# Performance work log

Hardware: AMD Instinct MI355X
Metric: run time of the kernel (lower is better)

The kernel has to match this reference:

```python
import jax, jax.numpy as jnp
import numpy as np

N = 200000      # tweet nodes
E = 1600000     # edges
U = 20000       # users (num_users)
D = 64          # embedding_dimension1 == embedding_dimension2
NUMP, CATP = 20, 12
EPS = 0.1       # PyG FAConv default eps


def setup_inputs() -> dict:
    key = jax.random.key(0)
    ks = jax.random.split(key, 20)
    s = 0.05
    offs = jnp.sort(jax.random.randint(ks[3], (U + 1,), 0, N, dtype=jnp.int64))
    offs = offs.at[0].set(0).at[-1].set(N)
    return {
        "num_prop": jax.random.normal(ks[0], (N, NUMP), jnp.float32),
        "cat_prop": jax.random.normal(ks[1], (N, CATP), jnp.float32),
        "tweet_offsets": offs,
        "edge_index": jax.random.randint(ks[2], (2, E), 0, N, dtype=jnp.int64),
        "re_index": jax.random.randint(ks[4], (U,), 0, U, dtype=jnp.int64),
        "W_num": jax.random.normal(ks[5], (NUMP, D // 2), jnp.float32) * s,
        "b_num": jnp.zeros((D // 2,), jnp.float32),
        "W_cat": jax.random.normal(ks[6], (CATP, D // 2), jnp.float32) * s,
        "b_cat": jnp.zeros((D // 2,), jnp.float32),
        "W_tog": jax.random.normal(ks[7], (D, D), jnp.float32) * s,
        "b_tog": jnp.zeros((D,), jnp.float32),
        "att_l": jax.random.normal(ks[8], (D,), jnp.float32) * s,
        "att_r": jax.random.normal(ks[9], (D,), jnp.float32) * s,
        "W_f1": jax.random.normal(ks[10], (D, D // 2), jnp.float32) * s,
        "b_f1": jnp.zeros((D // 2,), jnp.float32),
        "W_lab": jax.random.normal(ks[11], (D // 2, 2), jnp.float32) * s,
        "b_lab": jnp.zeros((2,), jnp.float32),
    }


def reference(num_prop, cat_prop, tweet_offsets, edge_index, re_index,
              W_num, b_num, W_cat, b_cat, W_tog, b_tog,
              att_l, att_r, W_f1, b_f1, W_lab, b_lab):
    n = num_prop.shape[0]
    lrelu = jax.nn.leaky_relu  # slope 0.01, matches nn.LeakyReLU default

    num = lrelu(num_prop @ W_num + b_num)
    cat = lrelu(cat_prop @ W_cat + b_cat)
    x = lrelu(jnp.concatenate([num, cat], axis=1) @ W_tog + b_tog)  # [N, D]

    # gcn_norm with self-loops (PyG FAConv default normalize=True, add_self_loops=True)
    loop = jnp.arange(n, dtype=edge_index.dtype)
    src = jnp.concatenate([edge_index[0], loop])
    dst = jnp.concatenate([edge_index[1], loop])
    deg = jax.ops.segment_sum(jnp.ones(src.shape[0], jnp.float32), dst, num_segments=n)
    dinv = jnp.where(deg > 0, deg ** -0.5, 0.0)
    norm = dinv[src] * dinv[dst]  # [E+N]

    def faconv(h, h0):
        # alpha_e = tanh(att_l . h[src] + att_r . h[dst]); out_i = sum_e norm_e * alpha_e * h[src_e]
        al = h @ att_l
        ar = h @ att_r
        alpha = jnp.tanh(al[src] + ar[dst]) * norm
        agg = jax.ops.segment_sum(h[src] * alpha[:, None], dst, num_segments=n)
        return agg + EPS * h0

    x1 = faconv(x, x)      # dropout is identity in eval mode
    x2 = faconv(x1, x)
    x2 = jnp.sqrt(x2 ** 2 + 1e-8)

    # ragged per-user segment sum from CSR offsets (replaces python loop+slice)
    nseg = tweet_offsets.shape[0] - 1
    seg = jnp.searchsorted(tweet_offsets, jnp.arange(n), side='right') - 1
    seg = jnp.clip(seg, 0, nseg - 1)
    x3 = jax.ops.segment_sum(x2, seg, num_segments=nseg)  # [U, D]

    x3 = x3[re_index]
    h = lrelu(x3 @ W_f1 + b_f1)
    return h @ W_lab + b_lab
```

## Files before the change

kernel.cpp:

```cpp
#include <hip/hip_runtime.h>
#include <hip/hip_bf16.h>

#define LRELU(v) ((v) > 0.0f ? (v) : 0.01f * (v))
#define EPS 0.1f

#define BSHIFT  9
#define BSIZE   512
#define BIN_EPB 2048
#define BIN_CAP 6144

typedef __attribute__((ext_vector_type(8))) short bf16x8;
typedef __attribute__((ext_vector_type(4))) float f32x4;

__device__ __forceinline__ float fast_tanh(float v)
{
    float e = __expf(2.0f * v);
    return 1.0f - 2.0f * __builtin_amdgcn_rcpf(e + 1.0f);
}

__device__ __forceinline__ float bf2f(unsigned short h)
{
    return __uint_as_float(((unsigned int)h) << 16);
}
__device__ __forceinline__ unsigned short f2bf(float f)
{
    unsigned int u = __float_as_uint(f);
    u += 0x7FFFu + ((u >> 16) & 1u);
    return (unsigned short)(u >> 16);
}

__global__ void k_prep(const float* __restrict__ W_num, const float* __restrict__ W_cat,
                       const float* __restrict__ W_tog,
                       unsigned short* __restrict__ Wb, unsigned short* __restrict__ Wb1)
{
    int t = threadIdx.x;
    for (int i = t; i < 8 * 512; i += 256) {
        int tile = i >> 9;
        int kt   = tile >> 2, nt = tile & 3;
        int lane = (i >> 3) & 63;
        int j    = i & 7;
        int k    = kt * 32 + (lane >> 4) * 8 + j;
        int n    = nt * 16 + (lane & 15);
        Wb[i] = f2bf(W_tog[k * 64 + n]);
    }
    for (int i = t; i < 4 * 512; i += 256) {
        int nt   = i >> 9;
        int lane = (i >> 3) & 63;
        int j    = i & 7;
        int k    = (lane >> 4) * 8 + j;
        int n    = nt * 16 + (lane & 15);
        float w;
        if (n < 32) w = (k < 20)  ? W_num[k * 32 + n]              : 0.0f;
        else        w = (k >= 20) ? W_cat[(k - 20) * 32 + (n - 32)] : 0.0f;
        Wb1[i] = f2bf(w);
    }
}

__global__ void __launch_bounds__(256)
k_feat(const float* __restrict__ num_prop,
       const float* __restrict__ cat_prop,
       const unsigned short* __restrict__ Wb1,
       const float* __restrict__ b_num, const float* __restrict__ b_cat,
       const unsigned short* __restrict__ Wb, const float* __restrict__ b_tog,
       const float* __restrict__ att_l, const float* __restrict__ att_r,
       unsigned short* __restrict__ xb,
       float* __restrict__ al, float* __restrict__ ar, int N)
{
    __shared__ unsigned short in_lds[64][40];
    __shared__ unsigned short mid[64][72];

    int tid  = threadIdx.x;
    int lane = tid & 63;
    int w    = tid >> 6;
    int blockStart = blockIdx.x * 64;

    for (int i = tid; i < 64 * 20; i += 256) {
        int node = i / 20, k = i % 20;
        int n = min(blockStart + node, N - 1);
        in_lds[node][k] = f2bf(num_prop[(size_t)n * 20 + k]);
    }
    for (int i = tid; i < 64 * 12; i += 256) {
        int node = i / 12, k = i % 12;
        int n = min(blockStart + node, N - 1);
        in_lds[node][20 + k] = f2bf(cat_prop[(size_t)n * 12 + k]);
    }
    __syncthreads();

    int q   = lane >> 4;
    int c16 = lane & 15;

    bf16x8 ain = *(const bf16x8*)&in_lds[w * 16 + c16][q * 8];
    #pragma unroll
    for (int nt = 0; nt < 4; nt++) {
        bf16x8 b = *(const bf16x8*)&Wb1[nt * 512 + lane * 8];
        f32x4 acc = {0.0f, 0.0f, 0.0f, 0.0f};
        acc = __builtin_amdgcn_mfma_f32_16x16x32_bf16(ain, b, acc, 0, 0, 0);
        int   ch   = nt * 16 + c16;
        float bias = (ch < 32) ? b_num[ch] : b_cat[ch - 32];
        #pragma unroll
        for (int r = 0; r < 4; r++) {
            float s = acc[r] + bias;
            s = LRELU(s);
            mid[w * 16 + q * 4 + r][ch] = f2bf(s);
        }
    }

    bf16x8 a0 = *(const bf16x8*)&mid[w * 16 + c16][q * 8];
    bf16x8 a1 = *(const bf16x8*)&mid[w * 16 + c16][32 + q * 8];

    float pal[4] = {0, 0, 0, 0};
    float par[4] = {0, 0, 0, 0};

    #pragma unroll
    for (int nt = 0; nt < 4; nt++) {
        bf16x8 b0 = *(const bf16x8*)&Wb[(0 * 4 + nt) * 512 + lane * 8];
        bf16x8 b1 = *(const bf16x8*)&Wb[(1 * 4 + nt) * 512 + lane * 8];
        f32x4 acc = {0.0f, 0.0f, 0.0f, 0.0f};
        acc = __builtin_amdgcn_mfma_f32_16x16x32_bf16(a0, b0, acc, 0, 0, 0);
        acc = __builtin_amdgcn_mfma_f32_16x16x32_bf16(a1, b1, acc, 0, 0, 0);

        int   ch  = nt * 16 + c16;
        float bt  = b_tog[ch];
        float atl = att_l[ch];
        float atr = att_r[ch];
        #pragma unroll
        for (int r = 0; r < 4; r++) {
            float s = acc[r] + bt;
            s = LRELU(s);
            int n = blockStart + w * 16 + q * 4 + r;
            if (n < N) xb[(size_t)n * 64 + ch] = f2bf(s);
            pal[r] = fmaf(s, atl, pal[r]);
            par[r] = fmaf(s, atr, par[r]);
        }
    }

    #pragma unroll
    for (int r = 0; r < 4; r++) {
        float pl = pal[r], pr = par[r];
        #pragma unroll
        for (int off = 8; off > 0; off >>= 1) {
            pl += __shfl_xor(pl, off);
            pr += __shfl_xor(pr, off);
        }
        int n = blockStart + w * 16 + q * 4 + r;
        if (c16 == 0 && n < N) { al[n] = pl; ar[n] = pr; }
    }
}

__global__ void k_bin(const int* __restrict__ src, const int* __restrict__ dst,
                      int* __restrict__ bucket_cnt,
                      int2* __restrict__ buckets, int E, int NB)
{
    __shared__ int  hist[BSIZE];
    __shared__ int  lbase[BSIZE];
    __shared__ int  gbase[BSIZE];
    __shared__ int2 stage[BIN_EPB];

    int tid  = threadIdx.x;
    int base = blockIdx.x * BIN_EPB;

    hist[tid] = 0;
    __syncthreads();

    int s[4], d[4], rk[4];
    #pragma unroll
    for (int k = 0; k < 4; k++) {
        int e = base + k * BSIZE + tid;
        s[k] = -1;
        if (e < E) {
            s[k] = src[e];
            d[k] = dst[e];
            rk[k] = atomicAdd(&hist[d[k] >> BSHIFT], 1);
        }
    }
    __syncthreads();

    int v = hist[tid];
    lbase[tid] = v;
    __syncthreads();
    for (int off = 1; off < BSIZE; off <<= 1) {
        int t = (tid >= off) ? lbase[tid - off] : 0;
        __syncthreads();
        lbase[tid] += t;
        __syncthreads();
    }
    int incl = lbase[tid];
    __syncthreads();
    lbase[tid] = incl - v;
    if (tid < NB && v > 0) gbase[tid] = atomicAdd(&bucket_cnt[tid], v);
    __syncthreads();

    #pragma unroll
    for (int k = 0; k < 4; k++) {
        if (s[k] >= 0) {
            int b = d[k] >> BSHIFT;
            stage[lbase[b] + rk[k]] = make_int2(s[k], d[k]);
        }
    }
    __syncthreads();

    int tot = min(BIN_EPB, E - base);
    for (int i = tid; i < tot; i += BSIZE) {
        int2 p = stage[i];
        int b = p.y >> BSHIFT;
        buckets[(size_t)b * BIN_CAP + gbase[b] + (i - lbase[b])] = p;
    }
}

__global__ void k_degScan(const int2* __restrict__ buckets, const int* __restrict__ bucket_cnt,
                          int* __restrict__ deg, int* __restrict__ row_start,
                          int* __restrict__ bucketTot, int N)
{
    __shared__ int cnt[BSIZE];
    __shared__ int sc[BSIZE];
    int b   = blockIdx.x;
    int tid = threadIdx.x;
    cnt[tid] = 0;
    __syncthreads();

    int ecnt = bucket_cnt[b];
    const int2* bp = buckets + (size_t)b * BIN_CAP;
    for (int i = tid; i < ecnt; i += BSIZE)
        atomicAdd(&cnt[bp[i].y & (BSIZE - 1)], 1);
    __syncthreads();

    int d = cnt[tid];
    int p = (d + 7) & ~7;
    sc[tid] = p;
    __syncthreads();
    for (int off = 1; off < BSIZE; off <<= 1) {
        int t = (tid >= off) ? sc[tid - off] : 0;
        __syncthreads();
        sc[tid] += t;
        __syncthreads();
    }
    int incl = sc[tid];

    int n = b * BSIZE + tid;
    if (n < N) {
        deg[n]       = d;
        row_start[n] = incl - p;
    }
    if (tid == BSIZE - 1) bucketTot[b] = incl;
}

__global__ void k_scan2(int* __restrict__ bucketTot, int nb)
{
    __shared__ int sh[BSIZE];
    int tid = threadIdx.x;
    int v = (tid < nb) ? bucketTot[tid] : 0;
    sh[tid] = v;
    __syncthreads();
    for (int off = 1; off < BSIZE; off <<= 1) {
        int t = (tid >= off) ? sh[tid - off] : 0;
        __syncthreads();
        sh[tid] += t;
        __syncthreads();
    }
    if (tid < nb) bucketTot[tid] = sh[tid] - v;
}

__global__ void k_scan3(int* __restrict__ row_start, const int* __restrict__ bucketTot,
                        const int* __restrict__ deg,
                        const float* __restrict__ al, float2* __restrict__ ald1,
                        int* __restrict__ srcs, float* __restrict__ alphas,
                        const int* __restrict__ offs, int* __restrict__ seg,
                        int N, int U)
{
    int i = blockIdx.x * blockDim.x + threadIdx.x;
    if (i >= N) return;
    int s0 = row_start[i] + bucketTot[i >> BSHIFT];
    row_start[i] = s0;
    int cnt  = deg[i];
    int cntp = (cnt + 7) & ~7;
    for (int k = cnt; k < cntp; k++) {
        srcs[s0 + k]   = 0;
        alphas[s0 + k] = 0.0f;
    }
    float dv = 1.0f / sqrtf((float)cnt + 1.0f);
    ald1[i]  = make_float2(al[i], dv);

    int lo = 0, hi = U;
    while (lo < hi) {
        int mid = (lo + hi) >> 1;
        if (offs[mid] <= i) lo = mid + 1; else hi = mid;
    }
    seg[i] = min(max(lo - 1, 0), U - 1);
}

__global__ void k_fill2(const int2* __restrict__ buckets, const int* __restrict__ bucket_cnt,
                        const int* __restrict__ row_start,
                        const float2* __restrict__ ald, const float* __restrict__ arr,
                        int* __restrict__ srcs, float* __restrict__ alphas)
{
    __shared__ int cur[BSIZE];
    int b   = blockIdx.x;
    int tid = threadIdx.x;
    cur[tid] = 0;
    __syncthreads();

    int cnt = bucket_cnt[b];
    const int2* bp = buckets + (size_t)b * BIN_CAP;
    for (int i = tid; i < cnt; i += BSIZE) {
        int2 p = bp[i];
        int r = p.y & (BSIZE - 1);
        int o = atomicAdd(&cur[r], 1);
        int pos = row_start[p.y] + o;
        float2 as = ald[p.x];
        float2 ad = ald[p.y];
        srcs[pos]   = p.x;
        alphas[pos] = fast_tanh(as.x + arr[p.y]) * as.y * ad.y;
    }
}

__global__ void k_alphaN(const int* __restrict__ srcs,
                         const int* __restrict__ row_start, const int* __restrict__ deg,
                         const float2* __restrict__ ald, const float* __restrict__ arr,
                         float* __restrict__ alphas, int N)
{
    int n = blockIdx.x * blockDim.x + threadIdx.x;
    if (n >= N) return;
    int   s0   = row_start[n];
    int   cnt  = deg[n];
    int   cntp = (cnt + 7) & ~7;
    float arn  = arr[n];
    float di   = ald[n].y;
    int k = 0;
    for (; k < cnt; k++) {
        int s = srcs[s0 + k];
        float2 as = ald[s];
        alphas[s0 + k] = fast_tanh(as.x + arn) * as.y * di;
    }
    for (; k < cntp; k++) alphas[s0 + k] = 0.0f;
}

__global__ void k_gather1(const int* __restrict__ srcs, const float* __restrict__ alphas,
                          const int* __restrict__ row_start, const int* __restrict__ deg,
                          const unsigned short* __restrict__ xb,
                          const float2* __restrict__ ald1, const float* __restrict__ ar,
                          const float* __restrict__ att_l, const float* __restrict__ att_r,
                          unsigned short* __restrict__ h1b, float2* __restrict__ ald2,
                          float* __restrict__ ar2, int N)
{
    int lane = threadIdx.x & 63;
    int n    = __builtin_amdgcn_readfirstlane(blockIdx.x * 4 + (threadIdx.x >> 6));
    if (n >= N) return;

    int    s0   = row_start[n];
    int    cnt  = deg[n];
    int    cntp = (cnt + 7) & ~7;
    float2 self = ald1[n];
    float  di   = self.y;
    float  arn  = ar[n];

    float acc = 0.0f;
    for (int j = 0; j < cntp; j += 8) {
        int sv[8]; float av[8], vv[8];
        #pragma unroll
        for (int t = 0; t < 8; t++) {
            sv[t] = srcs[s0 + j + t];
            av[t] = alphas[s0 + j + t];
        }
        #pragma unroll
        for (int t = 0; t < 8; t++) vv[t] = bf2f(xb[(size_t)sv[t] * 64 + lane]);
        #pragma unroll
        for (int t = 0; t < 8; t++) acc = fmaf(vv[t], av[t], acc);
    }

    float selfa = fast_tanh(self.x + arn) * di * di;
    float xnl   = bf2f(xb[(size_t)n * 64 + lane]);
    float v     = acc + (selfa + EPS) * xnl;

    float pl = v * att_l[lane];
    float pr = v * att_r[lane];
    #pragma unroll
    for (int off = 32; off > 0; off >>= 1) {
        pl += __shfl_down(pl, off);
        pr += __shfl_down(pr, off);
    }
    h1b[(size_t)n * 64 + lane] = f2bf(v);
    if (lane == 0) { ald2[n] = make_float2(pl, di); ar2[n] = pr; }
}

__global__ void k_gather2(const int* __restrict__ srcs, const float* __restrict__ alphas,
                          const int* __restrict__ row_start, const int* __restrict__ deg,
                          const unsigned short* __restrict__ h1b,
                          const unsigned short* __restrict__ xb,
                          const float2* __restrict__ ald2, const float* __restrict__ ar2,
                          const int* __restrict__ seg,
                          float* __restrict__ x3, int N)
{
    int lane = threadIdx.x & 63;
    int c0   = __builtin_amdgcn_readfirstlane(blockIdx.x * 4 + (threadIdx.x >> 6)) * 4;
    if (c0 >= N) return;
    int nend = min(c0 + 4, N);

    float uacc = 0.0f;
    int   useg = seg[c0];

    for (int n = c0; n < nend; n++) {
        int sg = seg[n];
        if (sg != useg) {
            atomicAdd(&x3[(size_t)useg * 64 + lane], uacc);
            uacc = 0.0f;
            useg = sg;
        }

        int    s0   = row_start[n];
        int    cnt  = deg[n];
        int    cntp = (cnt + 7) & ~7;
        float2 self = ald2[n];
        float  di   = self.y;
        float  arn  = ar2[n];

        float acc = 0.0f;
        for (int j = 0; j < cntp; j += 8) {
            int sv[8]; float av[8], vv[8];
            #pragma unroll
            for (int t = 0; t < 8; t++) {
                sv[t] = srcs[s0 + j + t];
                av[t] = alphas[s0 + j + t];
            }
            #pragma unroll
            for (int t = 0; t < 8; t++) vv[t] = bf2f(h1b[(size_t)sv[t] * 64 + lane]);
            #pragma unroll
            for (int t = 0; t < 8; t++) acc = fmaf(vv[t], av[t], acc);
        }

        float selfa = fast_tanh(self.x + arn) * di * di;
        float h1l   = bf2f(h1b[(size_t)n * 64 + lane]);
        float xnl   = bf2f(xb[(size_t)n * 64 + lane]);
        float v = acc + selfa * h1l + EPS * xnl;
        uacc += sqrtf(v * v + 1e-8f);
    }
    atomicAdd(&x3[(size_t)useg * 64 + lane], uacc);
}

__global__ void __launch_bounds__(256)
k_head(const float* __restrict__ x3, const int* __restrict__ re_index,
       const float* __restrict__ W_f1, const float* __restrict__ b_f1,
       const float* __restrict__ W_lab, const float* __restrict__ b_lab,
       float* __restrict__ out, int U)
{
    __shared__ float wf[64][32];
    __shared__ float wl[32][2];

    int tid = threadIdx.x;
    for (int i = tid; i < 64 * 32; i += 256) wf[i >> 5][i & 31] = W_f1[i];
    if (tid < 64) wl[tid >> 1][tid & 1] = W_lab[tid];
    __syncthreads();

    int u = blockIdx.x * blockDim.x + tid;
    if (u >= U) return;

    int r = re_index[u];
    const float* y = x3 + (size_t)r * 64;

    float s[32];
    #pragma unroll
    for (int j = 0; j < 32; j++) s[j] = b_f1[j];

    for (int k = 0; k < 64; k++) {
        float yk = y[k];
        #pragma unroll
        for (int j = 0; j < 32; j++) s[j] = fmaf(yk, wf[k][j], s[j]);
    }

    float o0 = b_lab[0], o1 = b_lab[1];
    #pragma unroll
    for (int j = 0; j < 32; j++) {
        float t = LRELU(s[j]);
        o0 = fmaf(t, wl[j][0], o0);
        o1 = fmaf(t, wl[j][1], o1);
    }
    out[(size_t)u * 2 + 0] = o0;
    out[(size_t)u * 2 + 1] = o1;
}

extern "C" void kernel_launch(void* const* d_in, const int* in_sizes, int n_in,
                              void* d_out, int out_size, void* d_ws, size_t ws_size,
                              hipStream_t stream)
{
    const float* num_prop = (const float*)d_in[0];
    const float* cat_prop = (const float*)d_in[1];
    const int*   offs     = (const int*)d_in[2];
    const int*   edge     = (const int*)d_in[3];
    const int*   re_index = (const int*)d_in[4];
    const float* W_num    = (const float*)d_in[5];
    const float* b_num    = (const float*)d_in[6];
    const float* W_cat    = (const float*)d_in[7];
    const float* b_cat    = (const float*)d_in[8];
    const float* W_tog    = (const float*)d_in[9];
    const float* b_tog    = (const float*)d_in[10];
    const float* att_l    = (const float*)d_in[11];
    const float* att_r    = (const float*)d_in[12];
    const float* W_f1     = (const float*)d_in[13];
    const float* b_f1     = (const float*)d_in[14];
    const float* W_lab    = (const float*)d_in[15];
    const float* b_lab    = (const float*)d_in[16];

    const int N = in_sizes[0] / 20;
    const int E = in_sizes[3] / 2;
    const int U = in_sizes[4];

    const int* src = edge;
    const int* dst = edge + E;

    const int    NB      = (N + BSIZE - 1) >> BSHIFT;
    const size_t srcsCap = (size_t)E + 7ull * (size_t)N + 64;

    float* ws = (float*)d_ws;
    size_t off = 0;
    unsigned short* xb  = (unsigned short*)(ws + off); off += (size_t)N * 32;
    unsigned short* h1b = (unsigned short*)(ws + off); off += (size_t)N * 32;
    float2* ald1 = (float2*)(ws + off); off += (size_t)N * 2;
    float2* ald2 = (float2*)(ws + off); off += (size_t)N * 2;
    int2*   buckets = (int2*)(ws + off); off += (size_t)NB * BIN_CAP * 2;
    float*  al   = ws + off; off += N;
    float*  ar   = ws + off; off += N;
    float*  ar2  = ws + off; off += N;
    float*  x3   = ws + off; off += (size_t)U * 64;
    unsigned short* Wb  = (unsigned short*)(ws + off); off += 2048;
    unsigned short* Wb1 = (unsigned short*)(ws + off); off += 1024;
    int*    deg        = (int*)(ws + off); off += N;
    int*    row_start  = (int*)(ws + off); off += N;
    int*    seg        = (int*)(ws + off); off += N;
    int*    bucket_cnt = (int*)(ws + off); off += NB;
    int*    bucketTot  = (int*)(ws + off); off += BSIZE;
    int*    srcs       = (int*)(ws + off); off += srcsCap;
    float*  alphas     = (float*)(ws + off); off += srcsCap;

    hipMemsetAsync(bucket_cnt, 0, (size_t)NB * 4, stream);
    hipMemsetAsync(x3, 0, (size_t)U * 64 * 4, stream);

    const int nbN4  = (N + 3) / 4;
    const int nbC   = (N + 15) / 16;
    const int nbN   = (N + 255) / 256;
    const int nbBin = (E + BIN_EPB - 1) / BIN_EPB;

    k_prep<<<1, 256, 0, stream>>>(W_num, W_cat, W_tog, Wb, Wb1);

    k_feat<<<(N + 63) / 64, 256, 0, stream>>>(num_prop, cat_prop, Wb1, b_num, b_cat,
                                              Wb, b_tog, att_l, att_r, xb, al, ar, N);

    k_bin<<<nbBin, BSIZE, 0, stream>>>(src, dst, bucket_cnt, buckets, E, NB);

    k_degScan<<<NB, BSIZE, 0, stream>>>(buckets, bucket_cnt, deg, row_start, bucketTot, N);
    k_scan2<<<1, BSIZE, 0, stream>>>(bucketTot, NB);
    k_scan3<<<nbN, 256, 0, stream>>>(row_start, bucketTot, deg, al, ald1,
                                     srcs, alphas, offs, seg, N, U);

    k_fill2<<<NB, BSIZE, 0, stream>>>(buckets, bucket_cnt, row_start, ald1, ar,
                                      srcs, alphas);

    k_gather1<<<nbN4, 256, 0, stream>>>(srcs, alphas, row_start, deg, xb, ald1, ar,
                                        att_l, att_r, h1b, ald2, ar2, N);

    k_alphaN<<<nbN, 256, 0, stream>>>(srcs, row_start, deg, ald2, ar2, alphas, N);
    k_gather2<<<nbC, 256, 0, stream>>>(srcs, alphas, row_start, deg, h1b, xb,
                                       ald2, ar2, seg, x3, N);

    k_head<<<(U + 255) / 256, 256, 0, stream>>>(x3, re_index, W_f1, b_f1, W_lab, b_lab,
                                                (float*)d_out, U);
}
```

Measured before the change: 383.3 us.

## Compute edge attention weights inside gather kernels instead of materializing alphas

Removes the per-edge alphas array and the k_alphaN kernel. k_fill2 now writes only source indices. Each gather wave computes up to 64 edge weights in parallel, one per lane, and broadcasts them with shuffles during accumulation. This drops the global write and read of alpha values and one kernel launch, at the cost of extra ald gathers and tanh work inside the gather loops.

```diff
diff --git a/kernel.cpp b/kernel.cpp
--- a/kernel.cpp
+++ b/kernel.cpp
@@ -263,7 +263,7 @@
 __global__ void k_scan3(int* __restrict__ row_start, const int* __restrict__ bucketTot,
                         const int* __restrict__ deg,
                         const float* __restrict__ al, float2* __restrict__ ald1,
-                        int* __restrict__ srcs, float* __restrict__ alphas,
+                        int* __restrict__ srcs,
                         const int* __restrict__ offs, int* __restrict__ seg,
                         int N, int U)
 {
@@ -273,10 +273,7 @@
     row_start[i] = s0;
     int cnt  = deg[i];
     int cntp = (cnt + 7) & ~7;
-    for (int k = cnt; k < cntp; k++) {
-        srcs[s0 + k]   = 0;
-        alphas[s0 + k] = 0.0f;
-    }
+    for (int k = cnt; k < cntp; k++) srcs[s0 + k] = 0;
     float dv = 1.0f / sqrtf((float)cnt + 1.0f);
     ald1[i]  = make_float2(al[i], dv);
 
@@ -290,8 +287,7 @@
 
 __global__ void k_fill2(const int2* __restrict__ buckets, const int* __restrict__ bucket_cnt,
                         const int* __restrict__ row_start,
-                        const float2* __restrict__ ald, const float* __restrict__ arr,
-                        int* __restrict__ srcs, float* __restrict__ alphas)
+                        int* __restrict__ srcs)
 {
     __shared__ int cur[BSIZE];
     int b   = blockIdx.x;
@@ -305,36 +301,11 @@
         int2 p = bp[i];
         int r = p.y & (BSIZE - 1);
         int o = atomicAdd(&cur[r], 1);
-        int pos = row_start[p.y] + o;
-        float2 as = ald[p.x];
-        float2 ad = ald[p.y];
-        srcs[pos]   = p.x;
-        alphas[pos] = fast_tanh(as.x + arr[p.y]) * as.y * ad.y;
-    }
-}
-
-__global__ void k_alphaN(const int* __restrict__ srcs,
-                         const int* __restrict__ row_start, const int* __restrict__ deg,
-                         const float2* __restrict__ ald, const float* __restrict__ arr,
-                         float* __restrict__ alphas, int N)
-{
-    int n = blockIdx.x * blockDim.x + threadIdx.x;
-    if (n >= N) return;
-    int   s0   = row_start[n];
-    int   cnt  = deg[n];
-    int   cntp = (cnt + 7) & ~7;
-    float arn  = arr[n];
-    float di   = ald[n].y;
-    int k = 0;
-    for (; k < cnt; k++) {
-        int s = srcs[s0 + k];
-        float2 as = ald[s];
-        alphas[s0 + k] = fast_tanh(as.x + arn) * as.y * di;
-    }
-    for (; k < cntp; k++) alphas[s0 + k] = 0.0f;
-}
-
-__global__ void k_gather1(const int* __restrict__ srcs, const float* __restrict__ alphas,
+        srcs[row_start[p.y] + o] = p.x;
+    }
+}
+
+__global__ void k_gather1(const int* __restrict__ srcs,
                           const int* __restrict__ row_start, const int* __restrict__ deg,
                           const unsigned short* __restrict__ xb,
                           const float2* __restrict__ ald1, const float* __restrict__ ar,
@@ -354,17 +325,24 @@
     float  arn  = ar[n];
 
     float acc = 0.0f;
-    for (int j = 0; j < cntp; j += 8) {
-        int sv[8]; float av[8], vv[8];
-        #pragma unroll
-        for (int t = 0; t < 8; t++) {
-            sv[t] = srcs[s0 + j + t];
-            av[t] = alphas[s0 + j + t];
-        }
-        #pragma unroll
-        for (int t = 0; t < 8; t++) vv[t] = bf2f(xb[(size_t)sv[t] * 64 + lane]);
-        #pragma unroll
-        for (int t = 0; t < 8; t++) acc = fmaf(vv[t], av[t], acc);
+    for (int jb = 0; jb < cntp; jb += 64) {
+        float a = 0.0f;
+        int   e = jb + lane;
+        if (e < cnt) {
+            int s = srcs[s0 + e];
+            float2 as = ald1[s];
+            a = fast_tanh(as.x + arn) * as.y * di;
+        }
+        int te = min(cntp - jb, 64);
+        for (int j = 0; j < te; j += 8) {
+            int sv[8]; float vv[8];
+            #pragma unroll
+            for (int t = 0; t < 8; t++) sv[t] = srcs[s0 + jb + j + t];
+            #pragma unroll
+            for (int t = 0; t < 8; t++) vv[t] = bf2f(xb[(size_t)sv[t] * 64 + lane]);
+            #pragma unroll
+            for (int t = 0; t < 8; t++) acc = fmaf(vv[t], __shfl(a, j + t), acc);
+        }
     }
 
     float selfa = fast_tanh(self.x + arn) * di * di;
@@ -382,7 +360,7 @@
     if (lane == 0) { ald2[n] = make_float2(pl, di); ar2[n] = pr; }
 }
 
-__global__ void k_gather2(const int* __restrict__ srcs, const float* __restrict__ alphas,
+__global__ void k_gather2(const int* __restrict__ srcs,
                           const int* __restrict__ row_start, const int* __restrict__ deg,
                           const unsigned short* __restrict__ h1b,
                           const unsigned short* __restrict__ xb,
@@ -414,17 +392,24 @@
         float  arn  = ar2[n];
 
         float acc = 0.0f;
-        for (int j = 0; j < cntp; j += 8) {
-            int sv[8]; float av[8], vv[8];
-            #pragma unroll
-            for (int t = 0; t < 8; t++) {
-                sv[t] = srcs[s0 + j + t];
-                av[t] = alphas[s0 + j + t];
+        for (int jb = 0; jb < cntp; jb += 64) {
+            float a = 0.0f;
+            int   e = jb + lane;
+            if (e < cnt) {
+                int s = srcs[s0 + e];
+                float2 as = ald2[s];
+                a = fast_tanh(as.x + arn) * as.y * di;
             }
-            #pragma unroll
-            for (int t = 0; t < 8; t++) vv[t] = bf2f(h1b[(size_t)sv[t] * 64 + lane]);
-            #pragma unroll
-            for (int t = 0; t < 8; t++) acc = fmaf(vv[t], av[t], acc);
+            int te = min(cntp - jb, 64);
+            for (int j = 0; j < te; j += 8) {
+                int sv[8]; float vv[8];
+                #pragma unroll
+                for (int t = 0; t < 8; t++) sv[t] = srcs[s0 + jb + j + t];
+                #pragma unroll
+                for (int t = 0; t < 8; t++) vv[t] = bf2f(h1b[(size_t)sv[t] * 64 + lane]);
+                #pragma unroll
+                for (int t = 0; t < 8; t++) acc = fmaf(vv[t], __shfl(a, j + t), acc);
+            }
         }
 
         float selfa = fast_tanh(self.x + arn) * di * di;
@@ -528,7 +513,6 @@
     int*    bucket_cnt = (int*)(ws + off); off += NB;
     int*    bucketTot  = (int*)(ws + off); off += BSIZE;
     int*    srcs       = (int*)(ws + off); off += srcsCap;
-    float*  alphas     = (float*)(ws + off); off += srcsCap;
 
     hipMemsetAsync(bucket_cnt, 0, (size_t)NB * 4, stream);
     hipMemsetAsync(x3, 0, (size_t)U * 64 * 4, stream);
@@ -548,16 +532,14 @@
     k_degScan<<<NB, BSIZE, 0, stream>>>(buckets, bucket_cnt, deg, row_start, bucketTot, N);
     k_scan2<<<1, BSIZE, 0, stream>>>(bucketTot, NB);
     k_scan3<<<nbN, 256, 0, stream>>>(row_start, bucketTot, deg, al, ald1,
-                                     srcs, alphas, offs, seg, N, U);
-
-    k_fill2<<<NB, BSIZE, 0, stream>>>(buckets, bucket_cnt, row_start, ald1, ar,
-                                      srcs, alphas);
-
-    k_gather1<<<nbN4, 256, 0, stream>>>(srcs, alphas, row_start, deg, xb, ald1, ar,
+                                     srcs, offs, seg, N, U);
+
+    k_fill2<<<NB, BSIZE, 0, stream>>>(buckets, bucket_cnt, row_start, srcs);
+
+    k_gather1<<<nbN4, 256, 0, stream>>>(srcs, row_start, deg, xb, ald1, ar,
                                         att_l, att_r, h1b, ald2, ar2, N);
 
-    k_alphaN<<<nbN, 256, 0, stream>>>(srcs, row_start, deg, ald2, ar2, alphas, N);
-    k_gather2<<<nbC, 256, 0, stream>>>(srcs, alphas, row_start, deg, h1b, xb,
+    k_gather2<<<nbC, 256, 0, stream>>>(srcs, row_start, deg, h1b, xb,
                                        ald2, ar2, seg, x3, N);
 
     k_head<<<(U + 255) / 256, 256, 0, stream>>>(x3, re_index, W_f1, b_f1, W_lab, b_lab,
```

Measured after the change: 352.1 us. 1.09x faster.
